# Kernel optimization log

Measured on AMD Instinct MI355X. Metric: run time of the kernel, lower is better.

## Reference

```python
import jax, jax.numpy as jnp
import numpy as np

B, N, K, C_IN, D = 4, 2048, 16, 480, 64
EPS = 1e-5


def _c1(x, w, b):
    # 1x1 Conv1d: x (B,C,N), w (O,C) -> (B,O,N)
    return jnp.einsum('oc,bcn->bon', w, x) + b[:, None]


def _c2(x, w, b):
    # 1x1 Conv2d: x (B,C,J,N), w (O,C) -> (B,O,J,N)
    return jnp.einsum('oc,bcjn->bojn', w, x) + b[:, None, None]


def _bn(x, g, b):
    # eval-mode BatchNorm2d with running_mean=0, running_var=1
    return x * (g / jnp.sqrt(1.0 + EPS))[:, None, None] + b[:, None, None]


def _mlp_res(x, w1, b1, w2, b2, ws, bs):
    return _c1(jax.nn.relu(_c1(x, w1, b1)), w2, b2) + _c1(x, ws, bs)


def _group(f, idx):
    # f (B,C,N), idx (B,K,N) int -> out[b,c,j,n] = f[b,c,idx[b,j,n]]  -> (B,C,K,N)
    return jax.vmap(lambda ff, ii: ff[:, ii])(f, idx)


def _knn_idx(xyz):
    # xyz (B,3,N) -> idx (B,K,N), excluding the self point (nearest neighbor)
    pts = xyz.transpose(0, 2, 1)  # (B,N,3)
    sq = jnp.sum(pts * pts, -1)
    d2 = sq[:, :, None] + sq[:, None, :] - 2.0 * jnp.einsum('bnd,bmd->bnm', pts, pts)
    _, idx = jax.lax.top_k(-d2, K + 1)  # (B,N,K+1), nearest first
    return idx.transpose(0, 2, 1)[:, 1:, :]  # drop self -> (B,K,N)


def _forward(idx, feature, xyz, bt1_w, bt1_b, bt2_w, bt2_b, bts_w, bts_b,
             q_w, q_b, k_w, k_b, v_w, v_b,
             fd1_w, fd1_b, fd_g, fd_bb, fd2_w, fd2_b,
             fg1_w, fg1_b, fg_g, fg_bb, fg2_w, fg2_b,
             at_w, at_b, m41_w, m41_b, m42_w, m42_b):
    x = _mlp_res(feature, bt1_w, bt1_b, bt2_w, bt2_b, bts_w, bts_b)  # (B,64,N)
    q = _c1(x, q_w, q_b)
    k = _c1(x, k_w, k_b)
    v = _c1(x, v_w, v_b)

    group_xyz = _group(xyz, idx)                       # (B,3,K,N)
    rel_xyz = xyz[:, :, None, :] - group_xyz           # (B,3,K,N)
    pos_enc = _c2(jax.nn.relu(_bn(_c2(rel_xyz, fd1_w, fd1_b), fd_g, fd_bb)), fd2_w, fd2_b)  # (B,64,K,N)

    k_local = _group(k, idx)                           # (B,64,K,N)
    v_local = _group(v, idx)
    qk_rel = q[:, :, None, :] - k_local
    attn = _c2(jax.nn.relu(_bn(_c2(qk_rel + pos_enc, fg1_w, fg1_b), fg_g, fg_bb)), fg2_w, fg2_b)  # (B,64,K,N)

    attn1 = attn.transpose(0, 1, 3, 2)                 # (B,64,N,K)
    # ConvTranspose2d(64,64,(4,1),(4,1)) with kernel==stride: out[b,o,4n+r,f] = sum_c x[b,c,n,f]*W[c,o,r] + bias[o]
    y = jnp.einsum('bcnf,cor->bonrf', attn1, at_w)
    y = y.reshape(y.shape[0], y.shape[1], -1, y.shape[4]) + at_b[None, :, None, None]  # (B,64,4N,K)
    attn = jax.nn.softmax(y, axis=1)

    value_rel = (v_local + pos_enc).transpose(0, 1, 3, 2)   # (B,64,N,K)
    value = jnp.repeat(value_rel, 4, axis=2)                # nearest upsample (4,1) -> (B,64,4N,K)

    res = jnp.einsum('bmnf,bmnf->bmn', attn, value)         # (B,64,4N)
    identity = jnp.repeat(x, 4, axis=2)                     # nearest upsample x4 -> (B,64,4N)
    res = res + identity
    completion = _c1(jax.nn.relu(_c1(res, m41_w, m41_b)), m42_w, m42_b)  # (B,3,4N)
    return completion, res


def setup_inputs() -> dict:
    key = jax.random.key(0)
    ks = jax.random.split(key, 24)
    i = iter(range(24))

    def w(shape):
        return (jax.random.normal(ks[next(i)], shape, dtype=jnp.float32) * 0.05)

    z = lambda n: jnp.zeros((n,), jnp.float32)
    o = lambda n: jnp.ones((n,), jnp.float32)
    return {
        'feature': jax.random.normal(ks[next(i)], (B, C_IN, N), dtype=jnp.float32),
        'xyz': jax.random.normal(ks[next(i)], (B, 3, N), dtype=jnp.float32),
        'bt1_w': w((D, C_IN)), 'bt1_b': z(D),
        'bt2_w': w((D, D)), 'bt2_b': z(D),
        'bts_w': w((D, C_IN)), 'bts_b': z(D),
        'q_w': w((D, D)), 'q_b': z(D),
        'k_w': w((D, D)), 'k_b': z(D),
        'v_w': w((D, D)), 'v_b': z(D),
        'fd1_w': w((D, 3)), 'fd1_b': z(D), 'fd_g': o(D), 'fd_bb': z(D),
        'fd2_w': w((D, D)), 'fd2_b': z(D),
        'fg1_w': w((4 * D, D)), 'fg1_b': z(4 * D), 'fg_g': o(4 * D), 'fg_bb': z(4 * D),
        'fg2_w': w((D, 4 * D)), 'fg2_b': z(D),
        'at_w': w((D, D, 4)), 'at_b': z(D),
        'm41_w': w((D, D)), 'm41_b': z(D),
        'm42_w': w((3, D)), 'm42_b': z(3),
    }


def reference(feature, xyz, bt1_w, bt1_b, bt2_w, bt2_b, bts_w, bts_b,
              q_w, q_b, k_w, k_b, v_w, v_b,
              fd1_w, fd1_b, fd_g, fd_bb, fd2_w, fd2_b,
              fg1_w, fg1_b, fg_g, fg_bb, fg2_w, fg2_b,
              at_w, at_b, m41_w, m41_b, m42_w, m42_b):
    idx = _knn_idx(xyz)
    return _forward(idx, feature, xyz, bt1_w, bt1_b, bt2_w, bt2_b, bts_w, bts_b,
                    q_w, q_b, k_w, k_b, v_w, v_b,
                    fd1_w, fd1_b, fd_g, fd_bb, fd2_w, fd2_b,
                    fg1_w, fg1_b, fg_g, fg_bb, fg2_w, fg2_b,
                    at_w, at_b, m41_w, m41_b, m42_w, m42_b)
```

## Files before the change

### kernel.cpp

```cpp
#include <hip/hip_runtime.h>

#define B_ 4
#define N_ 2048
#define K_ 16
#define CIN_ 480
#define UPN_ 8192
#define M_ (B_*N_*K_)
#define MX_ (B_*N_)
#define KCAP 448

typedef unsigned int u32;
typedef unsigned short u16;
typedef unsigned long long u64;
typedef __attribute__((ext_vector_type(8))) short short8;
typedef __attribute__((ext_vector_type(4))) float f32x4;

#define DEV static __device__ __forceinline__

#define WAVE_WAIT() do{ asm volatile("s_waitcnt lgkmcnt(0)" ::: "memory"); \
                        __builtin_amdgcn_sched_barrier(0); }while(0)

DEV float b2f(u16 h){ return __uint_as_float(((u32)h)<<16); }
DEV u16 f2b(float f){
  u32 u = __float_as_uint(f);
  u32 r = u + 0x7fffu + ((u>>16)&1u);
  return (u16)(r>>16);
}
DEV u32 cvtpk(float a, float b){
  u32 r; asm("v_cvt_pk_bf16_f32 %0, %1, %2" : "=v"(r) : "v"(a), "v"(b));
  return r;
}
DEV u64 cvtpk4(float a, float b, float c, float d){
  return (u64)cvtpk(a,b) | ((u64)cvtpk(c,d)<<32);
}
DEV bool detect_bf(const void* fg){ return ((((const u32*)fg)[0]) & 0xFFFFu) == 0x3F80u; }
DEV float ld(const void* p, int i, bool bf){
  return bf ? b2f(((const u16*)p)[i]) : ((const float*)p)[i];
}
DEV u64 makekey(float d2, int m){
  u32 bits = __float_as_uint(d2);
  bits = (bits & 0x80000000u) ? ~bits : (bits | 0x80000000u);
  return ((u64)bits<<32) | (u32)m;
}
DEV int swz64 (int row, int colByte){ return row*128 + (colByte ^ ((row&7)<<4)); }
DEV int swz128(int row, int colByte){ return row*256 + (colByte ^ ((row&7)<<4)); }

__global__ __launch_bounds__(256) void convert_kernel(const void* __restrict__ xyz,
    const void* __restrict__ fg, float* __restrict__ fxyz)
{
  bool bf = detect_bf(fg);
  const int XT = B_*3*N_;
  for(int i = blockIdx.x*256+threadIdx.x; i < XT; i += gridDim.x*256)
    fxyz[i] = bf ? b2f(((const u16*)xyz)[i]) : ((const float*)xyz)[i];
}

__global__ __launch_bounds__(256) void transpose_kernel(const void* __restrict__ feature,
    const void* __restrict__ fg, u16* __restrict__ fxbT)
{
  __shared__ u16 s[32][34];
  bool bf = detect_bf(fg);
  int ntile = blockIdx.x, ctile = blockIdx.y, b = blockIdx.z;
  int tx = threadIdx.x & 31, ty = threadIdx.x >> 5;
  u64 base = (u64)b*CIN_*N_;
  #pragma unroll
  for(int r=0;r<4;r++){
    int c = ctile*32 + ty + r*8;
    int n = ntile*32 + tx;
    u64 i = base + (u64)c*N_ + n;
    s[ty + r*8][tx] = bf ? ((const u16*)feature)[i] : f2b(((const float*)feature)[i]);
  }
  __syncthreads();
  #pragma unroll
  for(int r=0;r<4;r++){
    int nl = ty + r*8;
    int n = ntile*32 + nl;
    fxbT[(u64)b*N_*CIN_ + (u64)n*CIN_ + ctile*32 + tx] = s[tx][nl];
  }
}

__global__ __launch_bounds__(256) void prep_kernel(
    const void* __restrict__ bt1_w, const void* __restrict__ bt1_b,
    const void* __restrict__ bt2_w, const void* __restrict__ bt2_b,
    const void* __restrict__ bts_w, const void* __restrict__ bts_b,
    const void* __restrict__ q_w, const void* __restrict__ q_b,
    const void* __restrict__ k_w, const void* __restrict__ k_b,
    const void* __restrict__ v_w, const void* __restrict__ v_b,
    const void* __restrict__ fd1_w, const void* __restrict__ fd1_b,
    const void* __restrict__ fd_g, const void* __restrict__ fd_bb,
    const void* __restrict__ fd2_w, const void* __restrict__ fd2_b,
    const void* __restrict__ fg1_w, const void* __restrict__ fg1_b,
    const void* __restrict__ fg_g, const void* __restrict__ fg_bb,
    const void* __restrict__ fg2_w, const void* __restrict__ fg2_b,
    const void* __restrict__ at_w, const void* __restrict__ at_b,
    const void* __restrict__ m41_w, const void* __restrict__ m41_b,
    const void* __restrict__ m42_w, const void* __restrict__ m42_b,
    float* __restrict__ W, u16* __restrict__ WB)
{
  int t = blockIdx.x*256 + threadIdx.x;
  bool bf = detect_bf(fd_g);
  const float inv = 0.9999950000374997f;
  if(t < 30720){ int c=t>>6, o=t&63; W[t] = ld(bt1_w,o*CIN_+c,bf); return; } t -= 30720;
  if(t < 30720){ int c=t>>6, o=t&63; W[30720+t] = ld(bts_w,o*CIN_+c,bf); return; } t -= 30720;
  if(t < 4096){ int c=t>>6, o=t&63; W[61440+t] = ld(bt2_w,o*64+c,bf); return; } t -= 4096;
  if(t < 4096){ int c=t>>6, o=t&63; W[65536+t] = ld(q_w,o*64+c,bf); return; } t -= 4096;
  if(t < 4096){ int c=t>>6, o=t&63; W[69632+t] = ld(k_w,o*64+c,bf); return; } t -= 4096;
  if(t < 4096){ int c=t>>6, o=t&63; W[73728+t] = ld(v_w,o*64+c,bf); return; } t -= 4096;
  if(t < 256){
    int o=t>>2, j=t&3; float s = ld(fd_g,o,bf)*inv;
    W[77824+t] = (j<3) ? s*ld(fd1_w,o*3+j,bf) : (s*ld(fd1_b,o,bf) + ld(fd_bb,o,bf));
    return;
  } t -= 256;
  if(t < 4096){ int o=t>>6, m=t&63; W[78080+t] = ld(fd2_w,m*64+o,bf); return; } t -= 4096;
  if(t < 16384){ int o=t>>6; float s=ld(fg_g,o,bf)*inv; W[82176+t] = s*ld(fg1_w,t,bf); return; } t -= 16384;
  if(t < 256){ float s=ld(fg_g,t,bf)*inv; W[98560+t] = s*ld(fg1_b,t,bf) + ld(fg_bb,t,bf); return; } t -= 256;
  if(t < 16384){ int o=t>>6, m=t&63; W[98816+t] = ld(fg2_w,m*256+o,bf); return; } t -= 16384;
  if(t < 16384){ int r=t>>12, rem=t&4095, o=rem>>6, c=rem&63;
                 W[115200+t] = ld(at_w,(c*64+o)*4+r,bf); return; } t -= 16384;
  if(t < 4096){ int m=t>>6, o=t&63; W[131584+t] = ld(m41_w,o*64+m,bf); return; } t -= 4096;
  if(t < 192){ W[135680+t] = ld(m42_w,t,bf); return; } t -= 192;
  if(t < 64){ W[135872+t] = ld(bt1_b,t,bf); return; } t -= 64;
  if(t < 64){ W[135936+t] = ld(bts_b,t,bf); return; } t -= 64;
  if(t < 64){ W[136000+t] = ld(bt2_b,t,bf); return; } t -= 64;
  if(t < 64){ W[136064+t] = ld(q_b,t,bf); return; } t -= 64;
  if(t < 64){ W[136128+t] = ld(k_b,t,bf); return; } t -= 64;
  if(t < 64){ W[136192+t] = ld(v_b,t,bf); return; } t -= 64;
  if(t < 64){ W[136256+t] = ld(fd2_b,t,bf); return; } t -= 64;
  if(t < 64){ W[136320+t] = ld(fg2_b,t,bf); return; } t -= 64;
  if(t < 64){ W[136384+t] = ld(at_b,t,bf); return; } t -= 64;
  if(t < 64){ W[136448+t] = ld(m41_b,t,bf); return; } t -= 64;
  if(t < 3){ W[136512+t] = ld(m42_b,t,bf); return; } t -= 3;
  if(t < 16384){ int o=t>>6; float s=ld(fg_g,o,bf)*inv; WB[t] = f2b(s*ld(fg1_w,t,bf)); return; } t -= 16384;
  if(t < 16384){ WB[16384+t] = f2b(ld(fg2_w,t,bf)); return; } t -= 16384;
  if(t < 16384){ int j=t>>6, c=t&63;
                 WB[32768+t] = f2b(ld(at_w,(c*64+(j&63))*4+(j>>6),bf)); return; } t -= 16384;
  if(t < 256){ W[136576+t] = ld(at_b,t&63,bf); return; } t -= 256;
  if(t < 4096){ WB[49152+t] = f2b(ld(fd2_w,t,bf)); return; } t -= 4096;
  if(t < 30720){ WB[53248+t] = f2b(ld(bt1_w,t,bf)); return; } t -= 30720;
  if(t < 30720){ WB[83968+t] = f2b(ld(bts_w,t,bf)); return; } t -= 30720;
  if(t < 4096){ WB[114688+t] = f2b(ld(bt2_w,t,bf)); return; } t -= 4096;
  if(t < 4096){ WB[118784+t] = f2b(ld(q_w,t,bf)); return; } t -= 4096;
  if(t < 4096){ WB[122880+t] = f2b(ld(k_w,t,bf)); return; } t -= 4096;
  if(t < 4096){ WB[126976+t] = f2b(ld(v_w,t,bf)); return; }
}

__global__ __launch_bounds__(256) void knn_kernel(const float* __restrict__ fxyz,
                                                  int* __restrict__ idx)
{
  __shared__ float px[N_], py[N_], pz[N_], sq[N_];
  __shared__ u64 sbuf[4][KCAP];
  __shared__ u64 smin[4][64];
  __shared__ int scnt[4][64];
  __shared__ u64 stau[4];
  int b = blockIdx.y;
  const float* xb = fxyz + (u64)b*3*N_;
  for(int i=threadIdx.x;i<N_;i+=256){
    float xx=xb[i], yy=xb[N_+i], zz=xb[2*N_+i];
    px[i]=xx; py[i]=yy; pz[i]=zz; sq[i]=xx*xx+yy*yy+zz*zz;
  }
  __syncthreads();
  int w = threadIdx.x>>6, l = threadIdx.x&63;
  int q = blockIdx.x*4 + w;
  float qx=px[q], qy=py[q], qz=pz[q], qs=sq[q];
  float d2c[32];
  u64 best=~0ull;
  #pragma unroll
  for(int j=0;j<32;j++){
    int m = l*32 + ((j+l)&31);
    float d2 = (qs+sq[m]) - 2.0f*(qx*px[m]+qy*py[m]+qz*pz[m]);
    d2c[j]=d2;
    u64 key = makekey(d2, m);
    best = key<best ? key : best;
  }
  smin[w][l]=best;
  __syncthreads();
  {
    int rank=0;
    for(int i=0;i<64;i++) rank += (smin[w][i] < best);
    if(rank==16) stau[w] = best;
  }
  __syncthreads();
  u64 tau = stau[w];
  int myc=0;
  #pragma unroll
  for(int j=0;j<32;j++){
    int m = l*32 + ((j+l)&31);
    myc += (makekey(d2c[j], m) <= tau);
  }
  scnt[w][l]=myc;
  __syncthreads();
  int off=0, tot=0;
  for(int i=0;i<64;i++){
    int c = scnt[w][i];
    tot += c;
    off += (i<l) ? c : 0;
  }
  #pragma unroll
  for(int j=0;j<32;j++){
    int m = l*32 + ((j+l)&31);
    u64 key = makekey(d2c[j], m);
    if(key<=tau && off<KCAP){ sbuf[w][off]=key; off++; }
  }
  __syncthreads();
  if(tot>KCAP) tot=KCAP;
  for(int p=l; p<tot; p+=64){
    u64 kk = sbuf[w][p];
    int rk=0;
    for(int i=0;i<tot;i++) rk += (sbuf[w][i] < kk);
    if(rk>=1 && rk<17) idx[(b*K_+(rk-1))*N_+q] = ((int)(kk & 0xffffffffu)) & (N_-1);
  }
}

__global__ __launch_bounds__(256) void gemm480_mfma(const u16* __restrict__ A,
    const u16* __restrict__ Wt, const float* __restrict__ bias,
    u16* __restrict__ hout, float* __restrict__ xsout)
{
  int tid=threadIdx.x, w=tid>>6, lane=tid&63;
  int rbase=(blockIdx.x*4+w)*64;
  int cbase=blockIdx.y*64;
  int lr=lane&15, lk=(lane>>4)*8;
  f32x4 acc[4][4];
  #pragma unroll
  for(int i=0;i<4;i++)
    #pragma unroll
    for(int j=0;j<4;j++) acc[i][j]=(f32x4){0.f,0.f,0.f,0.f};
  for(int kc=0;kc<CIN_;kc+=32){
    short8 a[4], bb[4];
    #pragma unroll
    for(int ti=0;ti<4;ti++)
      a[ti] = *(const short8*)(A + (u64)(rbase+ti*16+lr)*CIN_ + kc + lk);
    #pragma unroll
    for(int tj=0;tj<4;tj++)
      bb[tj] = *(const short8*)(Wt + (u64)(cbase+tj*16+lr)*CIN_ + kc + lk);
    #pragma unroll
    for(int ti=0;ti<4;ti++)
      #pragma unroll
      for(int tj=0;tj<4;tj++)
        acc[ti][tj] = __builtin_amdgcn_mfma_f32_16x16x32_bf16(a[ti], bb[tj], acc[ti][tj], 0,0,0);
  }
  int rq=(lane>>4)*4;
  #pragma unroll
  for(int ti=0;ti<4;ti++)
    #pragma unroll
    for(int tj=0;tj<4;tj++){
      int col = cbase + tj*16 + lr;
      float bv = bias[col];
      #pragma unroll
      for(int reg=0;reg<4;reg++){
        u64 row = rbase + ti*16 + rq + reg;
        float vv = acc[ti][tj][reg] + bv;
        if(blockIdx.y==0) hout[row*64 + col] = f2b(fmaxf(vv,0.f));
        else              xsout[row*64 + (col-64)] = vv;
      }
    }
}

__global__ __launch_bounds__(256) void x_mfma(const u16* __restrict__ A,
    const u16* __restrict__ Wt, const float* __restrict__ bias,
    const float* __restrict__ xs, float* __restrict__ x, u16* __restrict__ xb)
{
  int tid=threadIdx.x, w=tid>>6, lane=tid&63;
  int rbase=(blockIdx.x*4+w)*64;
  int lr=lane&15, lk=(lane>>4)*8;
  f32x4 acc[4][4];
  #pragma unroll
  for(int i=0;i<4;i++)
    #pragma unroll
    for(int j=0;j<4;j++) acc[i][j]=(f32x4){0.f,0.f,0.f,0.f};
  for(int kc=0;kc<64;kc+=32){
    short8 a[4], bb[4];
    #pragma unroll
    for(int ti=0;ti<4;ti++)
      a[ti] = *(const short8*)(A + (u64)(rbase+ti*16+lr)*64 + kc + lk);
    #pragma unroll
    for(int tj=0;tj<4;tj++)
      bb[tj] = *(const short8*)(Wt + (u64)(tj*16+lr)*64 + kc + lk);
    #pragma unroll
    for(int ti=0;ti<4;ti++)
      #pragma unroll
      for(int tj=0;tj<4;tj++)
        acc[ti][tj] = __builtin_amdgcn_mfma_f32_16x16x32_bf16(a[ti], bb[tj], acc[ti][tj], 0,0,0);
  }
  int rq=(lane>>4)*4;
  #pragma unroll
  for(int ti=0;ti<4;ti++)
    #pragma unroll
    for(int tj=0;tj<4;tj++){
      int col = tj*16 + lr;
      float bv = bias[col];
      #pragma unroll
      for(int reg=0;reg<4;reg++){
        u64 row = rbase + ti*16 + rq + reg;
        float vv = acc[ti][tj][reg] + bv + xs[row*64+col];
        x[row*64+col] = vv;
        xb[row*64+col] = f2b(vv);
      }
    }
}

__global__ __launch_bounds__(256) void qkv_mfma(const u16* __restrict__ A,
    const u16* __restrict__ Wt, const float* __restrict__ bias, float* __restrict__ qkv)
{
  int tid=threadIdx.x, w=tid>>6, lane=tid&63;
  int rbase=(blockIdx.x*4+w)*64;
  int cbase=blockIdx.y*64;
  int lr=lane&15, lk=(lane>>4)*8;
  f32x4 acc[4][4];
  #pragma unroll
  for(int i=0;i<4;i++)
    #pragma unroll
    for(int j=0;j<4;j++) acc[i][j]=(f32x4){0.f,0.f,0.f,0.f};
  for(int kc=0;kc<64;kc+=32){
    short8 a[4], bb[4];
    #pragma unroll
    for(int ti=0;ti<4;ti++)
      a[ti] = *(const short8*)(A + (u64)(rbase+ti*16+lr)*64 + kc + lk);
    #pragma unroll
    for(int tj=0;tj<4;tj++)
      bb[tj] = *(const short8*)(Wt + (u64)(cbase+tj*16+lr)*64 + kc + lk);
    #pragma unroll
    for(int ti=0;ti<4;ti++)
      #pragma unroll
      for(int tj=0;tj<4;tj++)
        acc[ti][tj] = __builtin_amdgcn_mfma_f32_16x16x32_bf16(a[ti], bb[tj], acc[ti][tj], 0,0,0);
  }
  int rq=(lane>>4)*4;
  #pragma unroll
  for(int ti=0;ti<4;ti++)
    #pragma unroll
    for(int tj=0;tj<4;tj++){
      int col = cbase + tj*16 + lr;
      float bv = bias[col];
      #pragma unroll
      for(int reg=0;reg<4;reg++){
        u64 row = rbase + ti*16 + rq + reg;
        qkv[row*192 + col] = acc[ti][tj][reg] + bv;
      }
    }
}

__global__ __launch_bounds__(256) void fused_chain(
    const int* __restrict__ idx, const float* __restrict__ fxyz,
    const float* __restrict__ qkv, const float* __restrict__ x,
    const float* __restrict__ fd1f,
    const u16* __restrict__ Wfd2, const float* __restrict__ bfd2,
    const u16* __restrict__ Wfg1, const float* __restrict__ bfg1,
    const u16* __restrict__ Wfg2, const float* __restrict__ bfg2,
    const u16* __restrict__ Wat,  const float* __restrict__ bat,
    const void* __restrict__ det, void* __restrict__ out)
{
  __shared__ alignas(16) unsigned char lds[32768];
  int tid = threadIdx.x;
  int w = tid>>6, lane = tid&63;
  int lr = lane&15, lk = (lane>>4)*8, rq = (lane>>4)*4;

  int erow = tid>>2, ecg = tid&3;
  int el = erow>>4, ef = erow&15;
  int bn_e = blockIdx.x*4 + el;
  int b_e = bn_e>>11, n_e = bn_e&(N_-1);
  int jn = idx[(b_e*K_+ef)*N_ + n_e] & (N_-1);

  {
    const float* xb = fxyz + (u64)b_e*3*N_;
    float rx = xb[n_e]      - xb[jn];
    float ry = xb[N_+n_e]   - xb[N_+jn];
    float rz = xb[2*N_+n_e] - xb[2*N_+jn];
    #pragma unroll
    for(int gg=0; gg<4; gg++){
      float tv[4];
      #pragma unroll
      for(int j=0;j<4;j++){
        f32x4 wv = *(const f32x4*)(fd1f + ((ecg*4+gg)*4+j)*4);
        tv[j] = fmaxf(wv[0]*rx + wv[1]*ry + wv[2]*rz + wv[3], 0.f);
      }
      *(u64*)(lds + swz64(erow, (ecg*4+gg)*8)) = cvtpk4(tv[0],tv[1],tv[2],tv[3]);
    }
  }
  __syncthreads();

  {
    f32x4 acc[4];
    #pragma unroll
    for(int i=0;i<4;i++) acc[i]=(f32x4){0.f,0.f,0.f,0.f};
    #pragma unroll
    for(int kc=0;kc<64;kc+=32){
      short8 wf = *(const short8*)(Wfd2 + (u64)(w*16+lr)*64 + kc + lk);
      #pragma unroll
      for(int ti=0;ti<4;ti++){
        short8 tf = *(const short8*)(lds + swz64(ti*16+lr, (kc+lk)*2));
        acc[ti] = __builtin_amdgcn_mfma_f32_16x16x32_bf16(wf, tf, acc[ti], 0,0,0);
      }
    }
    f32x4 b4 = *(const f32x4*)(bfd2 + w*16 + rq);
    #pragma unroll
    for(int ti=0;ti<4;ti++)
      *(u64*)(lds + 8192 + swz64(ti*16+lr, (w*16+rq)*2)) =
        cvtpk4(acc[ti][0]+b4[0], acc[ti][1]+b4[1], acc[ti][2]+b4[2], acc[ti][3]+b4[3]);
  }
  __syncthreads();

  {
    int mg = ecg*16;
    const float* qrow = qkv + (u64)(b_e*N_+n_e)*192 + mg;
    const float* krow = qkv + (u64)(b_e*N_+jn)*192 + 64 + mg;
    const float* vrow = qkv + (u64)(b_e*N_+jn)*192 + 128 + mg;
    #pragma unroll
    for(int g2=0; g2<4; g2++){
      f32x4 qv = *(const f32x4*)(qrow + g2*4);
      f32x4 kv = *(const f32x4*)(krow + g2*4);
      f32x4 vv = *(const f32x4*)(vrow + g2*4);
      int cb = (mg + g2*4)*2;
      u64 pw = *(const u64*)(lds + 8192 + swz64(erow, cb));
      float p0=b2f((u16)pw), p1=b2f((u16)(pw>>16)), p2=b2f((u16)(pw>>32)), p3=b2f((u16)(pw>>48));
      *(u64*)(lds + swz64(erow, cb)) =
        cvtpk4(qv[0]-kv[0]+p0, qv[1]-kv[1]+p1, qv[2]-kv[2]+p2, qv[3]-kv[3]+p3);
      *(u64*)(lds + 8192 + swz64(erow, cb)) =
        cvtpk4(vv[0]+p0, vv[1]+p1, vv[2]+p2, vv[3]+p3);
    }
  }
  __syncthreads();

  float vreg[16];
  #pragma unroll
  for(int f2=0; f2<16; f2++)
    vreg[f2] = b2f(*(const u16*)(lds + 8192 + swz64(w*16+f2, lane*2)));

  f32x4 gacc[4];
  #pragma unroll
  for(int i=0;i<4;i++) gacc[i]=(f32x4){0.f,0.f,0.f,0.f};
  #pragma unroll
  for(int half=0; half<2; half++){
    {
      f32x4 hacc[2][4];
      #pragma unroll
      for(int i=0;i<2;i++)
        #pragma unroll
        for(int j=0;j<4;j++) hacc[i][j]=(f32x4){0.f,0.f,0.f,0.f};
      #pragma unroll
      for(int kc=0;kc<64;kc+=32){
        short8 wf[2], af[4];
        #pragma unroll
        for(int ti=0;ti<2;ti++)
          wf[ti] = *(const short8*)(Wfg1 + (u64)(half*128 + w*32 + ti*16 + lr)*64 + kc + lk);
        #pragma unroll
        for(int tj=0;tj<4;tj++)
          af[tj] = *(const short8*)(lds + swz64(tj*16+lr, (kc+lk)*2));
        #pragma unroll
        for(int ti=0;ti<2;ti++)
          #pragma unroll
          for(int tj=0;tj<4;tj++)
            hacc[ti][tj] = __builtin_amdgcn_mfma_f32_16x16x32_bf16(wf[ti], af[tj], hacc[ti][tj], 0,0,0);
      }
      #pragma unroll
      for(int ti=0;ti<2;ti++){
        f32x4 b4 = *(const f32x4*)(bfg1 + half*128 + w*32 + ti*16 + rq);
        #pragma unroll
        for(int tj=0;tj<4;tj++){
          int row = tj*16 + lr;
          *(u64*)(lds + 16384 + swz128(row, (w*32+ti*16+rq)*2)) =
            cvtpk4(fmaxf(hacc[ti][tj][0]+b4[0],0.f), fmaxf(hacc[ti][tj][1]+b4[1],0.f),
                   fmaxf(hacc[ti][tj][2]+b4[2],0.f), fmaxf(hacc[ti][tj][3]+b4[3],0.f));
        }
      }
    }
    __syncthreads();
    #pragma unroll
    for(int kc=0;kc<128;kc+=32){
      short8 wf = *(const short8*)(Wfg2 + (u64)(w*16+lr)*256 + half*128 + kc + lk);
      #pragma unroll
      for(int tj=0;tj<4;tj++){
        short8 hf = *(const short8*)(lds + 16384 + swz128(tj*16+lr, (kc+lk)*2));
        gacc[tj] = __builtin_amdgcn_mfma_f32_16x16x32_bf16(wf, hf, gacc[tj], 0,0,0);
      }
    }
    __syncthreads();
  }

  {
    f32x4 b4 = *(const f32x4*)(bfg2 + w*16 + rq);
    #pragma unroll
    for(int tj=0;tj<4;tj++)
      *(u64*)(lds + swz64(tj*16+lr, (w*16+rq)*2)) =
        cvtpk4(gacc[tj][0]+b4[0], gacc[tj][1]+b4[1], gacc[tj][2]+b4[2], gacc[tj][3]+b4[3]);
  }
  __syncthreads();

  float aout[4];
  unsigned char* Lp = lds + 16384 + w*2048;
  #pragma unroll
  for(int r=0;r<4;r++){
    f32x4 acc[4];
    #pragma unroll
    for(int i=0;i<4;i++) acc[i]=(f32x4){0.f,0.f,0.f,0.f};
    #pragma unroll
    for(int kc=0;kc<64;kc+=32){
      short8 gf = *(const short8*)(lds + swz64(w*16+lr, (kc+lk)*2));
      #pragma unroll
      for(int ct=0;ct<4;ct++){
        short8 wf = *(const short8*)(Wat + (u64)(r*64 + ct*16 + lr)*64 + kc + lk);
        acc[ct] = __builtin_amdgcn_mfma_f32_16x16x32_bf16(wf, gf, acc[ct], 0,0,0);
      }
    }
    float yv[16];
    #pragma unroll
    for(int ct=0;ct<4;ct++){
      f32x4 b4 = *(const f32x4*)(bat + r*64 + ct*16 + rq);
      #pragma unroll
      for(int reg=0;reg<4;reg++) yv[ct*4+reg] = acc[ct][reg] + b4[reg];
    }
    float mx = yv[0];
    #pragma unroll
    for(int m=1;m<16;m++) mx = fmaxf(mx, yv[m]);
    mx = fmaxf(mx, __shfl_xor(mx, 16));
    mx = fmaxf(mx, __shfl_xor(mx, 32));
    float sm = 0.f;
    #pragma unroll
    for(int m=0;m<16;m++){ float e = __expf(yv[m]-mx); yv[m]=e; sm+=e; }
    sm += __shfl_xor(sm, 16);
    sm += __shfl_xor(sm, 32);
    float rinv = 1.0f/sm;
    #pragma unroll
    for(int ct=0;ct<4;ct++)
      *(u64*)(Lp + swz64(lr, (ct*16+rq)*2)) =
        cvtpk4(yv[ct*4+0]*rinv, yv[ct*4+1]*rinv, yv[ct*4+2]*rinv, yv[ct*4+3]*rinv);
    WAVE_WAIT();
    float a = 0.f;
    #pragma unroll
    for(int f2=0; f2<16; f2++)
      a += b2f(*(const u16*)(Lp + swz64(f2, lane*2))) * vreg[f2];
    aout[r] = a;
    WAVE_WAIT();
  }

  int bn = blockIdx.x*4 + w;
  int b = bn>>11, n = bn&(N_-1);
  float xv = x[(u64)bn*64 + lane];
  u64 off = 98304 + ((u64)(b*64+lane))*UPN_ + (u64)n*4;
  if(detect_bf(det)){
    *(u64*)((u16*)out + off) = cvtpk4(aout[0]+xv, aout[1]+xv, aout[2]+xv, aout[3]+xv);
  } else {
    f32x4 pk = {aout[0]+xv, aout[1]+xv, aout[2]+xv, aout[3]+xv};
    *(f32x4*)((float*)out + off) = pk;
  }
}

__global__ __launch_bounds__(256) void comp_kernel(
  const float* __restrict__ m41T, const float* __restrict__ m41b,
  const float* __restrict__ m42f, const float* __restrict__ m42b,
  const void* __restrict__ det, void* __restrict__ out)
{
  int t = blockIdx.x*256 + threadIdx.x;
  int un = t & (UPN_-1);
  int b = t >> 13;
  bool bf = detect_bf(det);
  float acc[64];
  #pragma unroll
  for(int o=0;o<64;o++) acc[o] = m41b[o];
  if(bf){
    const u16* rr = (const u16*)out + 98304 + (u64)b*64*UPN_ + un;
    for(int c=0;c<64;c++){
      float rv = b2f(rr[(u64)c*UPN_]);
      const float* w = m41T + c*64;
      #pragma unroll
      for(int o=0;o<64;o++) acc[o] += w[o]*rv;
    }
  } else {
    const float* rr = (const float*)out + 98304 + (u64)b*64*UPN_ + un;
    for(int c=0;c<64;c++){
      float rv = rr[(u64)c*UPN_];
      const float* w = m41T + c*64;
      #pragma unroll
      for(int o=0;o<64;o++) acc[o] += w[o]*rv;
    }
  }
  float c0=m42b[0], c1=m42b[1], c2=m42b[2];
  #pragma unroll
  for(int o=0;o<64;o++){
    float hv = fmaxf(acc[o],0.f);
    c0 += m42f[o]*hv; c1 += m42f[64+o]*hv; c2 += m42f[128+o]*hv;
  }
  u64 base = (u64)b*3*UPN_ + un;
  if(bf){
    u16* cp = (u16*)out;
    cp[base]=f2b(c0); cp[base+UPN_]=f2b(c1); cp[base+2*UPN_]=f2b(c2);
  } else {
    float* cp = (float*)out;
    cp[base]=c0; cp[base+UPN_]=c1; cp[base+2*UPN_]=c2;
  }
}

extern "C" void kernel_launch(void* const* d_in, const int* in_sizes, int n_in,
                              void* d_out, int out_size, void* d_ws, size_t ws_size,
                              hipStream_t stream)
{
  (void)in_sizes; (void)n_in; (void)out_size; (void)ws_size;
  const void* feature=d_in[0];
  const void* xyz   =d_in[1];
  const void* bt1_w =d_in[2];  const void* bt1_b=d_in[3];
  const void* bt2_w =d_in[4];  const void* bt2_b=d_in[5];
  const void* bts_w =d_in[6];  const void* bts_b=d_in[7];
  const void* q_w   =d_in[8];  const void* q_b =d_in[9];
  const void* k_w   =d_in[10]; const void* k_b =d_in[11];
  const void* v_w   =d_in[12]; const void* v_b =d_in[13];
  const void* fd1_w =d_in[14]; const void* fd1_b=d_in[15];
  const void* fd_g  =d_in[16]; const void* fd_bb=d_in[17];
  const void* fd2_w =d_in[18]; const void* fd2_b=d_in[19];
  const void* fg1_w =d_in[20]; const void* fg1_b=d_in[21];
  const void* fg_g  =d_in[22]; const void* fg_bb=d_in[23];
  const void* fg2_w =d_in[24]; const void* fg2_b=d_in[25];
  const void* at_w  =d_in[26]; const void* at_b =d_in[27];
  const void* m41_w =d_in[28]; const void* m41_b=d_in[29];
  const void* m42_w =d_in[30]; const void* m42_b=d_in[31];

  char* ws=(char*)d_ws;
  float* W   =(float*)(ws);
  u16*  WB   =(u16*)  (ws + 589824);
  int*  idx  =(int*)  (ws + 851968);
  float* x   =(float*)(ws + 1376256);
  float* qkv =(float*)(ws + 3473408);
  u16*  h    =(u16*)  (ws + 9764864);
  float* xs  =(float*)(ws + 10813440);
  u16*  xb   =(u16*)  (ws + 12910592);
  u16*  fxbT =(u16*)  (ws + 114622464);
  float* fxyz=(float*)(ws + 122486784);

  const float* W_fd1f = W+77824;
  const float* W_fg1fb= W+98560;
  const float* W_m41T = W+131584;
  const float* W_m42  = W+135680;
  const float* Wb_g480= W+135872;
  const float* Wb_bt2 = W+136000;
  const float* Wb_qkv = W+136064;
  const float* Wb_fd2 = W+136256;
  const float* Wb_fg2 = W+136320;
  const float* Wb_m41 = W+136448;
  const float* Wb_m42 = W+136512;
  const float* W_atb256 = W+136576;
  const u16* WB_fg1  = WB;
  const u16* WB_fg2  = WB+16384;
  const u16* WB_at   = WB+32768;
  const u16* WB_fd2  = WB+49152;
  const u16* WB_g480 = WB+53248;
  const u16* WB_bt2  = WB+114688;
  const u16* WB_qkv  = WB+118784;

  convert_kernel<<<96,256,0,stream>>>(xyz, fd_g, fxyz);
  prep_kernel<<<1047,256,0,stream>>>(bt1_w,bt1_b,bt2_w,bt2_b,bts_w,bts_b,q_w,q_b,k_w,k_b,
      v_w,v_b,fd1_w,fd1_b,fd_g,fd_bb,fd2_w,fd2_b,fg1_w,fg1_b,fg_g,fg_bb,fg2_w,fg2_b,
      at_w,at_b,m41_w,m41_b,m42_w,m42_b,W,WB);
  transpose_kernel<<<dim3(64,15,4),256,0,stream>>>(feature, fd_g, fxbT);
  knn_kernel<<<dim3(N_/4,B_),256,0,stream>>>(fxyz, idx);
  gemm480_mfma<<<dim3(MX_/256,2),256,0,stream>>>(fxbT, WB_g480, Wb_g480, h, xs);
  x_mfma<<<MX_/256,256,0,stream>>>(h, WB_bt2, Wb_bt2, xs, x, xb);
  qkv_mfma<<<dim3(MX_/256,3),256,0,stream>>>(xb, WB_qkv, Wb_qkv, qkv);
  fused_chain<<<B_*N_/4,256,0,stream>>>(idx, fxyz, qkv, x, W_fd1f,
      WB_fd2, Wb_fd2, WB_fg1, W_fg1fb, WB_fg2, Wb_fg2, WB_at, W_atb256, fd_g, d_out);
  comp_kernel<<<128,256,0,stream>>>(W_m41T, Wb_m41, W_m42, Wb_m42, fd_g, d_out);
}
```

Before: 296.7 us.

## Fuse xyz conversion into knn, shrink GEMM tiles, redistribute softmax, trim prep

Drops the separate xyz conversion kernel: knn now reads raw xyz and one block column writes the float copy. Stops prep from writing fp32 weight copies that are no longer read. Shrinks the three small MFMA GEMMs from 64-row to 16-row tiles per wave so more blocks launch. Reorganises the attention-transpose softmax in fused_chain so each wave computes a row slice and block-wide syncs share results through LDS. comp_kernel now uses 128-thread blocks with twice as many blocks. The trade-offs are lower per-wave data reuse in the GEMMs and extra __syncthreads plus a bf16 round trip of logits in the softmax.

```diff
diff --git a/kernel.cpp b/kernel.cpp
--- a/kernel.cpp
+++ b/kernel.cpp
@@ -17,9 +17,6 @@
 
 #define DEV static __device__ __forceinline__
 
-#define WAVE_WAIT() do{ asm volatile("s_waitcnt lgkmcnt(0)" ::: "memory"); \
-                        __builtin_amdgcn_sched_barrier(0); }while(0)
-
 DEV float b2f(u16 h){ return __uint_as_float(((u32)h)<<16); }
 DEV u16 f2b(float f){
   u32 u = __float_as_uint(f);
@@ -44,15 +41,6 @@
 }
 DEV int swz64 (int row, int colByte){ return row*128 + (colByte ^ ((row&7)<<4)); }
 DEV int swz128(int row, int colByte){ return row*256 + (colByte ^ ((row&7)<<4)); }
-
-__global__ __launch_bounds__(256) void convert_kernel(const void* __restrict__ xyz,
-    const void* __restrict__ fg, float* __restrict__ fxyz)
-{
-  bool bf = detect_bf(fg);
-  const int XT = B_*3*N_;
-  for(int i = blockIdx.x*256+threadIdx.x; i < XT; i += gridDim.x*256)
-    fxyz[i] = bf ? b2f(((const u16*)xyz)[i]) : ((const float*)xyz)[i];
-}
 
 __global__ __launch_bounds__(256) void transpose_kernel(const void* __restrict__ feature,
     const void* __restrict__ fg, u16* __restrict__ fxbT)
@@ -99,23 +87,22 @@
   int t = blockIdx.x*256 + threadIdx.x;
   bool bf = detect_bf(fd_g);
   const float inv = 0.9999950000374997f;
-  if(t < 30720){ int c=t>>6, o=t&63; W[t] = ld(bt1_w,o*CIN_+c,bf); return; } t -= 30720;
-  if(t < 30720){ int c=t>>6, o=t&63; W[30720+t] = ld(bts_w,o*CIN_+c,bf); return; } t -= 30720;
-  if(t < 4096){ int c=t>>6, o=t&63; W[61440+t] = ld(bt2_w,o*64+c,bf); return; } t -= 4096;
-  if(t < 4096){ int c=t>>6, o=t&63; W[65536+t] = ld(q_w,o*64+c,bf); return; } t -= 4096;
-  if(t < 4096){ int c=t>>6, o=t&63; W[69632+t] = ld(k_w,o*64+c,bf); return; } t -= 4096;
-  if(t < 4096){ int c=t>>6, o=t&63; W[73728+t] = ld(v_w,o*64+c,bf); return; } t -= 4096;
+  if(t < 30720) return; t -= 30720;
+  if(t < 30720) return; t -= 30720;
+  if(t < 4096) return; t -= 4096;
+  if(t < 4096) return; t -= 4096;
+  if(t < 4096) return; t -= 4096;
+  if(t < 4096) return; t -= 4096;
   if(t < 256){
     int o=t>>2, j=t&3; float s = ld(fd_g,o,bf)*inv;
     W[77824+t] = (j<3) ? s*ld(fd1_w,o*3+j,bf) : (s*ld(fd1_b,o,bf) + ld(fd_bb,o,bf));
     return;
   } t -= 256;
-  if(t < 4096){ int o=t>>6, m=t&63; W[78080+t] = ld(fd2_w,m*64+o,bf); return; } t -= 4096;
-  if(t < 16384){ int o=t>>6; float s=ld(fg_g,o,bf)*inv; W[82176+t] = s*ld(fg1_w,t,bf); return; } t -= 16384;
+  if(t < 4096) return; t -= 4096;
+  if(t < 16384) return; t -= 16384;
   if(t < 256){ float s=ld(fg_g,t,bf)*inv; W[98560+t] = s*ld(fg1_b,t,bf) + ld(fg_bb,t,bf); return; } t -= 256;
-  if(t < 16384){ int o=t>>6, m=t&63; W[98816+t] = ld(fg2_w,m*256+o,bf); return; } t -= 16384;
-  if(t < 16384){ int r=t>>12, rem=t&4095, o=rem>>6, c=rem&63;
-                 W[115200+t] = ld(at_w,(c*64+o)*4+r,bf); return; } t -= 16384;
+  if(t < 16384) return; t -= 16384;
+  if(t < 16384) return; t -= 16384;
   if(t < 4096){ int m=t>>6, o=t&63; W[131584+t] = ld(m41_w,o*64+m,bf); return; } t -= 4096;
   if(t < 192){ W[135680+t] = ld(m42_w,t,bf); return; } t -= 192;
   if(t < 64){ W[135872+t] = ld(bt1_b,t,bf); return; } t -= 64;
@@ -143,8 +130,8 @@
   if(t < 4096){ WB[126976+t] = f2b(ld(v_w,t,bf)); return; }
 }
 
-__global__ __launch_bounds__(256) void knn_kernel(const float* __restrict__ fxyz,
-                                                  int* __restrict__ idx)
+__global__ __launch_bounds__(256) void knn_kernel(const void* __restrict__ xyz,
+    const void* __restrict__ fg, float* __restrict__ fxyz, int* __restrict__ idx)
 {
   __shared__ float px[N_], py[N_], pz[N_], sq[N_];
   __shared__ u64 sbuf[4][KCAP];
@@ -152,10 +139,13 @@
   __shared__ int scnt[4][64];
   __shared__ u64 stau[4];
   int b = blockIdx.y;
-  const float* xb = fxyz + (u64)b*3*N_;
+  bool bf = detect_bf(fg);
+  int base = b*3*N_;
+  bool w0 = (blockIdx.x==0);
   for(int i=threadIdx.x;i<N_;i+=256){
-    float xx=xb[i], yy=xb[N_+i], zz=xb[2*N_+i];
+    float xx=ld(xyz,base+i,bf), yy=ld(xyz,base+N_+i,bf), zz=ld(xyz,base+2*N_+i,bf);
     px[i]=xx; py[i]=yy; pz[i]=zz; sq[i]=xx*xx+yy*yy+zz*zz;
+    if(w0){ fxyz[base+i]=xx; fxyz[base+N_+i]=yy; fxyz[base+2*N_+i]=zz; }
   }
   __syncthreads();
   int w = threadIdx.x>>6, l = threadIdx.x&63;
@@ -215,43 +205,33 @@
     u16* __restrict__ hout, float* __restrict__ xsout)
 {
   int tid=threadIdx.x, w=tid>>6, lane=tid&63;
-  int rbase=(blockIdx.x*4+w)*64;
+  int rbase=(blockIdx.x*4+w)*16;
   int cbase=blockIdx.y*64;
   int lr=lane&15, lk=(lane>>4)*8;
-  f32x4 acc[4][4];
-  #pragma unroll
-  for(int i=0;i<4;i++)
-    #pragma unroll
-    for(int j=0;j<4;j++) acc[i][j]=(f32x4){0.f,0.f,0.f,0.f};
+  f32x4 acc[4];
+  #pragma unroll
+  for(int j=0;j<4;j++) acc[j]=(f32x4){0.f,0.f,0.f,0.f};
   for(int kc=0;kc<CIN_;kc+=32){
-    short8 a[4], bb[4];
-    #pragma unroll
-    for(int ti=0;ti<4;ti++)
-      a[ti] = *(const short8*)(A + (u64)(rbase+ti*16+lr)*CIN_ + kc + lk);
-    #pragma unroll
-    for(int tj=0;tj<4;tj++)
-      bb[tj] = *(const short8*)(Wt + (u64)(cbase+tj*16+lr)*CIN_ + kc + lk);
-    #pragma unroll
-    for(int ti=0;ti<4;ti++)
-      #pragma unroll
-      for(int tj=0;tj<4;tj++)
-        acc[ti][tj] = __builtin_amdgcn_mfma_f32_16x16x32_bf16(a[ti], bb[tj], acc[ti][tj], 0,0,0);
+    short8 a = *(const short8*)(A + (u64)(rbase+lr)*CIN_ + kc + lk);
+    #pragma unroll
+    for(int tj=0;tj<4;tj++){
+      short8 bb = *(const short8*)(Wt + (u64)(cbase+tj*16+lr)*CIN_ + kc + lk);
+      acc[tj] = __builtin_amdgcn_mfma_f32_16x16x32_bf16(a, bb, acc[tj], 0,0,0);
+    }
   }
   int rq=(lane>>4)*4;
   #pragma unroll
-  for(int ti=0;ti<4;ti++)
-    #pragma unroll
-    for(int tj=0;tj<4;tj++){
-      int col = cbase + tj*16 + lr;
-      float bv = bias[col];
-      #pragma unroll
-      for(int reg=0;reg<4;reg++){
-        u64 row = rbase + ti*16 + rq + reg;
-        float vv = acc[ti][tj][reg] + bv;
-        if(blockIdx.y==0) hout[row*64 + col] = f2b(fmaxf(vv,0.f));
-        else              xsout[row*64 + (col-64)] = vv;
-      }
-    }
+  for(int tj=0;tj<4;tj++){
+    int col = cbase + tj*16 + lr;
+    float bv = bias[col];
+    #pragma unroll
+    for(int reg=0;reg<4;reg++){
+      u64 row = rbase + rq + reg;
+      float vv = acc[tj][reg] + bv;
+      if(blockIdx.y==0) hout[row*64 + col] = f2b(fmaxf(vv,0.f));
+      else              xsout[row*64 + (col-64)] = vv;
+    }
+  }
 }
 
 __global__ __launch_bounds__(256) void x_mfma(const u16* __restrict__ A,
@@ -259,83 +239,65 @@
     const float* __restrict__ xs, float* __restrict__ x, u16* __restrict__ xb)
 {
   int tid=threadIdx.x, w=tid>>6, lane=tid&63;
-  int rbase=(blockIdx.x*4+w)*64;
+  int rbase=(blockIdx.x*4+w)*16;
   int lr=lane&15, lk=(lane>>4)*8;
-  f32x4 acc[4][4];
-  #pragma unroll
-  for(int i=0;i<4;i++)
-    #pragma unroll
-    for(int j=0;j<4;j++) acc[i][j]=(f32x4){0.f,0.f,0.f,0.f};
+  f32x4 acc[4];
+  #pragma unroll
+  for(int j=0;j<4;j++) acc[j]=(f32x4){0.f,0.f,0.f,0.f};
+  #pragma unroll
   for(int kc=0;kc<64;kc+=32){
-    short8 a[4], bb[4];
-    #pragma unroll
-    for(int ti=0;ti<4;ti++)
-      a[ti] = *(const short8*)(A + (u64)(rbase+ti*16+lr)*64 + kc + lk);
-    #pragma unroll
-    for(int tj=0;tj<4;tj++)
-      bb[tj] = *(const short8*)(Wt + (u64)(tj*16+lr)*64 + kc + lk);
-    #pragma unroll
-    for(int ti=0;ti<4;ti++)
-      #pragma unroll
-      for(int tj=0;tj<4;tj++)
-        acc[ti][tj] = __builtin_amdgcn_mfma_f32_16x16x32_bf16(a[ti], bb[tj], acc[ti][tj], 0,0,0);
+    short8 a = *(const short8*)(A + (u64)(rbase+lr)*64 + kc + lk);
+    #pragma unroll
+    for(int tj=0;tj<4;tj++){
+      short8 bb = *(const short8*)(Wt + (u64)(tj*16+lr)*64 + kc + lk);
+      acc[tj] = __builtin_amdgcn_mfma_f32_16x16x32_bf16(a, bb, acc[tj], 0,0,0);
+    }
   }
   int rq=(lane>>4)*4;
   #pragma unroll
-  for(int ti=0;ti<4;ti++)
-    #pragma unroll
-    for(int tj=0;tj<4;tj++){
-      int col = tj*16 + lr;
-      float bv = bias[col];
-      #pragma unroll
-      for(int reg=0;reg<4;reg++){
-        u64 row = rbase + ti*16 + rq + reg;
-        float vv = acc[ti][tj][reg] + bv + xs[row*64+col];
-        x[row*64+col] = vv;
-        xb[row*64+col] = f2b(vv);
-      }
-    }
+  for(int tj=0;tj<4;tj++){
+    int col = tj*16 + lr;
+    float bv = bias[col];
+    #pragma unroll
+    for(int reg=0;reg<4;reg++){
+      u64 row = rbase + rq + reg;
+      float vv = acc[tj][reg] + bv + xs[row*64+col];
+      x[row*64+col] = vv;
+      xb[row*64+col] = f2b(vv);
+    }
+  }
 }
 
 __global__ __launch_bounds__(256) void qkv_mfma(const u16* __restrict__ A,
     const u16* __restrict__ Wt, const float* __restrict__ bias, float* __restrict__ qkv)
 {
   int tid=threadIdx.x, w=tid>>6, lane=tid&63;
-  int rbase=(blockIdx.x*4+w)*64;
+  int rbase=(blockIdx.x*4+w)*16;
   int cbase=blockIdx.y*64;
   int lr=lane&15, lk=(lane>>4)*8;
-  f32x4 acc[4][4];
-  #pragma unroll
-  for(int i=0;i<4;i++)
-    #pragma unroll
-    for(int j=0;j<4;j++) acc[i][j]=(f32x4){0.f,0.f,0.f,0.f};
+  f32x4 acc[4];
+  #pragma unroll
+  for(int j=0;j<4;j++) acc[j]=(f32x4){0.f,0.f,0.f,0.f};
+  #pragma unroll
   for(int kc=0;kc<64;kc+=32){
-    short8 a[4], bb[4];
-    #pragma unroll
-    for(int ti=0;ti<4;ti++)
-      a[ti] = *(const short8*)(A + (u64)(rbase+ti*16+lr)*64 + kc + lk);
-    #pragma unroll
-    for(int tj=0;tj<4;tj++)
-      bb[tj] = *(const short8*)(Wt + (u64)(cbase+tj*16+lr)*64 + kc + lk);
-    #pragma unroll
-    for(int ti=0;ti<4;ti++)
-      #pragma unroll
-      for(int tj=0;tj<4;tj++)
-        acc[ti][tj] = __builtin_amdgcn_mfma_f32_16x16x32_bf16(a[ti], bb[tj], acc[ti][tj], 0,0,0);
+    short8 a = *(const short8*)(A + (u64)(rbase+lr)*64 + kc + lk);
+    #pragma unroll
+    for(int tj=0;tj<4;tj++){
+      short8 bb = *(const short8*)(Wt + (u64)(cbase+tj*16+lr)*64 + kc + lk);
+      acc[tj] = __builtin_amdgcn_mfma_f32_16x16x32_bf16(a, bb, acc[tj], 0,0,0);
+    }
   }
   int rq=(lane>>4)*4;
   #pragma unroll
-  for(int ti=0;ti<4;ti++)
-    #pragma unroll
-    for(int tj=0;tj<4;tj++){
-      int col = cbase + tj*16 + lr;
-      float bv = bias[col];
-      #pragma unroll
-      for(int reg=0;reg<4;reg++){
-        u64 row = rbase + ti*16 + rq + reg;
-        qkv[row*192 + col] = acc[ti][tj][reg] + bv;
-      }
-    }
+  for(int tj=0;tj<4;tj++){
+    int col = cbase + tj*16 + lr;
+    float bv = bias[col];
+    #pragma unroll
+    for(int reg=0;reg<4;reg++){
+      u64 row = rbase + rq + reg;
+      qkv[row*192 + col] = acc[tj][reg] + bv;
+    }
+  }
 }
 
 __global__ __launch_bounds__(256) void fused_chain(
@@ -485,50 +447,68 @@
   __syncthreads();
 
   float aout[4];
-  unsigned char* Lp = lds + 16384 + w*2048;
+  int srow = tid>>2, sub = tid&3;
   #pragma unroll
   for(int r=0;r<4;r++){
-    f32x4 acc[4];
-    #pragma unroll
-    for(int i=0;i<4;i++) acc[i]=(f32x4){0.f,0.f,0.f,0.f};
-    #pragma unroll
-    for(int kc=0;kc<64;kc+=32){
-      short8 gf = *(const short8*)(lds + swz64(w*16+lr, (kc+lk)*2));
-      #pragma unroll
-      for(int ct=0;ct<4;ct++){
-        short8 wf = *(const short8*)(Wat + (u64)(r*64 + ct*16 + lr)*64 + kc + lk);
-        acc[ct] = __builtin_amdgcn_mfma_f32_16x16x32_bf16(wf, gf, acc[ct], 0,0,0);
+    {
+      f32x4 acc[4];
+      #pragma unroll
+      for(int i=0;i<4;i++) acc[i]=(f32x4){0.f,0.f,0.f,0.f};
+      #pragma unroll
+      for(int kc=0;kc<64;kc+=32){
+        short8 wf = *(const short8*)(Wat + (u64)(r*64 + w*16 + lr)*64 + kc + lk);
+        #pragma unroll
+        for(int tj=0;tj<4;tj++){
+          short8 gf = *(const short8*)(lds + swz64(tj*16+lr, (kc+lk)*2));
+          acc[tj] = __builtin_amdgcn_mfma_f32_16x16x32_bf16(wf, gf, acc[tj], 0,0,0);
+        }
       }
-    }
-    float yv[16];
-    #pragma unroll
-    for(int ct=0;ct<4;ct++){
-      f32x4 b4 = *(const f32x4*)(bat + r*64 + ct*16 + rq);
-      #pragma unroll
-      for(int reg=0;reg<4;reg++) yv[ct*4+reg] = acc[ct][reg] + b4[reg];
-    }
-    float mx = yv[0];
-    #pragma unroll
-    for(int m=1;m<16;m++) mx = fmaxf(mx, yv[m]);
-    mx = fmaxf(mx, __shfl_xor(mx, 16));
-    mx = fmaxf(mx, __shfl_xor(mx, 32));
-    float sm = 0.f;
-    #pragma unroll
-    for(int m=0;m<16;m++){ float e = __expf(yv[m]-mx); yv[m]=e; sm+=e; }
-    sm += __shfl_xor(sm, 16);
-    sm += __shfl_xor(sm, 32);
-    float rinv = 1.0f/sm;
-    #pragma unroll
-    for(int ct=0;ct<4;ct++)
-      *(u64*)(Lp + swz64(lr, (ct*16+rq)*2)) =
-        cvtpk4(yv[ct*4+0]*rinv, yv[ct*4+1]*rinv, yv[ct*4+2]*rinv, yv[ct*4+3]*rinv);
-    WAVE_WAIT();
-    float a = 0.f;
-    #pragma unroll
-    for(int f2=0; f2<16; f2++)
-      a += b2f(*(const u16*)(Lp + swz64(f2, lane*2))) * vreg[f2];
-    aout[r] = a;
-    WAVE_WAIT();
+      f32x4 b4 = *(const f32x4*)(bat + r*64 + w*16 + rq);
+      #pragma unroll
+      for(int tj=0;tj<4;tj++)
+        *(u64*)(lds + 16384 + swz64(tj*16+lr, (w*16+rq)*2)) =
+          cvtpk4(acc[tj][0]+b4[0], acc[tj][1]+b4[1], acc[tj][2]+b4[2], acc[tj][3]+b4[3]);
+    }
+    __syncthreads();
+    {
+      float yv[16];
+      uint4 pk0 = *(const uint4*)(lds + 16384 + swz64(srow, sub*32));
+      uint4 pk1 = *(const uint4*)(lds + 16384 + swz64(srow, sub*32 + 16));
+      yv[0]=__uint_as_float(pk0.x<<16); yv[1]=__uint_as_float(pk0.x&0xffff0000u);
+      yv[2]=__uint_as_float(pk0.y<<16); yv[3]=__uint_as_float(pk0.y&0xffff0000u);
+      yv[4]=__uint_as_float(pk0.z<<16); yv[5]=__uint_as_float(pk0.z&0xffff0000u);
+      yv[6]=__uint_as_float(pk0.w<<16); yv[7]=__uint_as_float(pk0.w&0xffff0000u);
+      yv[8]=__uint_as_float(pk1.x<<16); yv[9]=__uint_as_float(pk1.x&0xffff0000u);
+      yv[10]=__uint_as_float(pk1.y<<16); yv[11]=__uint_as_float(pk1.y&0xffff0000u);
+      yv[12]=__uint_as_float(pk1.z<<16); yv[13]=__uint_as_float(pk1.z&0xffff0000u);
+      yv[14]=__uint_as_float(pk1.w<<16); yv[15]=__uint_as_float(pk1.w&0xffff0000u);
+      float mx = yv[0];
+      #pragma unroll
+      for(int m=1;m<16;m++) mx = fmaxf(mx, yv[m]);
+      mx = fmaxf(mx, __shfl_xor(mx, 1));
+      mx = fmaxf(mx, __shfl_xor(mx, 2));
+      float sm = 0.f;
+      #pragma unroll
+      for(int m=0;m<16;m++){ float e = __expf(yv[m]-mx); yv[m]=e; sm+=e; }
+      sm += __shfl_xor(sm, 1);
+      sm += __shfl_xor(sm, 2);
+      float rinv = 1.0f/sm;
+      uint4 o0, o1;
+      o0.x = cvtpk(yv[0]*rinv, yv[1]*rinv);  o0.y = cvtpk(yv[2]*rinv, yv[3]*rinv);
+      o0.z = cvtpk(yv[4]*rinv, yv[5]*rinv);  o0.w = cvtpk(yv[6]*rinv, yv[7]*rinv);
+      o1.x = cvtpk(yv[8]*rinv, yv[9]*rinv);  o1.y = cvtpk(yv[10]*rinv, yv[11]*rinv);
+      o1.z = cvtpk(yv[12]*rinv, yv[13]*rinv); o1.w = cvtpk(yv[14]*rinv, yv[15]*rinv);
+      *(uint4*)(lds + 8192 + swz64(srow, sub*32))      = o0;
+      *(uint4*)(lds + 8192 + swz64(srow, sub*32 + 16)) = o1;
+    }
+    __syncthreads();
+    {
+      float a = 0.f;
+      #pragma unroll
+      for(int f2=0; f2<16; f2++)
+        a += b2f(*(const u16*)(lds + 8192 + swz64(w*16+f2, lane*2))) * vreg[f2];
+      aout[r] = a;
+    }
   }
 
   int bn = blockIdx.x*4 + w;
@@ -543,12 +523,12 @@
   }
 }
 
-__global__ __launch_bounds__(256) void comp_kernel(
+__global__ __launch_bounds__(128) void comp_kernel(
   const float* __restrict__ m41T, const float* __restrict__ m41b,
   const float* __restrict__ m42f, const float* __restrict__ m42b,
   const void* __restrict__ det, void* __restrict__ out)
 {
-  int t = blockIdx.x*256 + threadIdx.x;
+  int t = blockIdx.x*128 + threadIdx.x;
   int un = t & (UPN_-1);
   int b = t >> 13;
   bool bf = detect_bf(det);
@@ -643,16 +623,15 @@
   const u16* WB_bt2  = WB+114688;
   const u16* WB_qkv  = WB+118784;
 
-  convert_kernel<<<96,256,0,stream>>>(xyz, fd_g, fxyz);
   prep_kernel<<<1047,256,0,stream>>>(bt1_w,bt1_b,bt2_w,bt2_b,bts_w,bts_b,q_w,q_b,k_w,k_b,
       v_w,v_b,fd1_w,fd1_b,fd_g,fd_bb,fd2_w,fd2_b,fg1_w,fg1_b,fg_g,fg_bb,fg2_w,fg2_b,
       at_w,at_b,m41_w,m41_b,m42_w,m42_b,W,WB);
   transpose_kernel<<<dim3(64,15,4),256,0,stream>>>(feature, fd_g, fxbT);
-  knn_kernel<<<dim3(N_/4,B_),256,0,stream>>>(fxyz, idx);
-  gemm480_mfma<<<dim3(MX_/256,2),256,0,stream>>>(fxbT, WB_g480, Wb_g480, h, xs);
-  x_mfma<<<MX_/256,256,0,stream>>>(h, WB_bt2, Wb_bt2, xs, x, xb);
-  qkv_mfma<<<dim3(MX_/256,3),256,0,stream>>>(xb, WB_qkv, Wb_qkv, qkv);
+  knn_kernel<<<dim3(N_/4,B_),256,0,stream>>>(xyz, fd_g, fxyz, idx);
+  gemm480_mfma<<<dim3(MX_/64,2),256,0,stream>>>(fxbT, WB_g480, Wb_g480, h, xs);
+  x_mfma<<<MX_/64,256,0,stream>>>(h, WB_bt2, Wb_bt2, xs, x, xb);
+  qkv_mfma<<<dim3(MX_/64,3),256,0,stream>>>(xb, WB_qkv, Wb_qkv, qkv);
   fused_chain<<<B_*N_/4,256,0,stream>>>(idx, fxyz, qkv, x, W_fd1f,
       WB_fd2, Wb_fd2, WB_fg1, W_fg1fb, WB_fg2, Wb_fg2, WB_at, W_atb256, fd_g, d_out);
-  comp_kernel<<<128,256,0,stream>>>(W_m41T, Wb_m41, W_m42, Wb_m42, fd_g, d_out);
-}
+  comp_kernel<<<256,128,0,stream>>>(W_m41T, Wb_m41, W_m42, Wb_m42, fd_g, d_out);
+}
```

New measurement: 267.8 us. 9.7% less time.
